# Optimization experiments

Measured on AMD Instinct MI355X. Metric: run time of the kernel, lower is better.

The kernel has to match this reference:

```python
import jax, jax.numpy as jnp
import numpy as np

BSZ, S, F, K, PI = 32, 4096, 512, 4, 1


def setup_inputs() -> dict:
    key = jax.random.key(0)
    ks = jax.random.split(key, 5)
    x = jax.random.normal(ks[0], (BSZ, S, F), dtype=jnp.float32)
    s = 1.0 / np.float32(np.sqrt(F))
    Wu = jax.random.normal(ks[1], (F, F), dtype=jnp.float32) * s
    P = jax.random.normal(ks[2], (F // K, F), dtype=jnp.float32) * s
    Q = jax.random.normal(ks[3], (F, PI * F), dtype=jnp.float32) * s
    Bb = jax.random.normal(ks[4], (F // K, PI * F), dtype=jnp.float32) * 0.01
    return {"x": x, "Wu": Wu, "P": P, "Q": Q, "Bb": Bb}


def reference(x, Wu, P, Q, Bb):
    # x: [B, S, F]
    B_, S_, F_ = x.shape
    Fk = P.shape[0]          # F // k
    k = F_ // Fk
    piF = Q.shape[1]
    # Ux = relu(x @ Wu): [B, S, F]
    Ux = jax.nn.relu(jnp.einsum('bsf,fg->bsg', x, Wu))
    # KMaxPooling over sequence axis: transpose to [B, F, S], top_k -> [B, F, k]
    topv = jax.lax.top_k(jnp.transpose(Ux, (0, 2, 1)), k)[0]
    # original does a raw reshape [B, F, k] -> [B, k, F] (element order preserved)
    z = topv.reshape(B_, k, F_)
    # P is reshaped in call() from [F/k, F] to [F, F/k]
    P2 = P.reshape(F_, Fk)
    # diag(z_i) @ P2 == z_i[:, None] * P2 -> [B, k, F, F/k], then per-i reshape to [B, F/k, F]
    zp = (z[:, :, :, None] * P2[None, None, :, :]).reshape(B_, k, Fk, F_)
    # @ Q, bias add, relu: [B, k, F/k, pi*F]
    out = jax.nn.relu(jnp.einsum('bkmf,fq->bkmq', zp, Q) + Bb[None, None, :, :])
    # concat over k along axis 1 -> [B, F, pi*F]
    return out.reshape(B_, F_, piF)
```

## Files before the change

### kernel.cpp

```cpp
#include <hip/hip_runtime.h>

#define BSZ   32
#define SEQ   4096
#define FDIM  512
#define KTOP  4
#define FK    128
#define MTOT  (BSZ * SEQ)
#define NCHUNK 32

#define BM2  256
#define BN2  256
#define BK2  64
#define NKT  (FDIM / BK2)

typedef __attribute__((ext_vector_type(8))) short bf16x8;
typedef __attribute__((ext_vector_type(4))) float f32x4;
typedef __attribute__((ext_vector_type(8))) unsigned short u16x8;

typedef __attribute__((address_space(1))) void void_g;
typedef __attribute__((address_space(3))) void void_l;

static __device__ __forceinline__ void load_lds16(const void* g, void* l) {
  __builtin_amdgcn_global_load_lds((void_g*)g, (void_l*)l, 16, 0, 0);
}

static __device__ __forceinline__ unsigned short f2bf(float f) {
  unsigned int u = __float_as_uint(f);
  unsigned int r = (u + 0x7fffu + ((u >> 16) & 1u)) >> 16;
  return (unsigned short)r;
}

static __device__ __forceinline__ void sort2(float& a, float& b) {
  float mx = fmaxf(a, b), mn = fminf(a, b); a = mx; b = mn;
}
static __device__ __forceinline__ void sort4(float& a, float& b, float& c, float& d) {
  sort2(a, b); sort2(c, d); sort2(a, c); sort2(b, d); sort2(b, c);
}
static __device__ __forceinline__ void merge4(float& a, float& b, float& c, float& d,
                                              float e, float f, float g, float h) {
  float m0 = fmaxf(a, h), m1 = fmaxf(b, g), m2 = fmaxf(c, f), m3 = fmaxf(d, e);
  sort2(m0, m2); sort2(m1, m3); sort2(m0, m1); sort2(m2, m3);
  a = m0; b = m1; c = m2; d = m3;
}

__global__ __launch_bounds__(256) void cvt_wuT_kernel(const float* __restrict__ Wu,
                                                      unsigned short* __restrict__ WuT) {
  int nn = blockIdx.x;
  for (int k = threadIdx.x; k < FDIM; k += blockDim.x)
    WuT[(size_t)nn * FDIM + k] = f2bf(Wu[(size_t)k * FDIM + nn]);
}

__global__ __launch_bounds__(256) void compute_R_kernel(const float* __restrict__ P,
                                                        const float* __restrict__ Q,
                                                        float* __restrict__ R) {
  int g = blockIdx.y;
  int q = blockIdx.x * 256 + threadIdx.x;
  __shared__ float p2[FK];
  if (threadIdx.x < FK) p2[threadIdx.x] = P[(size_t)g * FK + threadIdx.x];
  __syncthreads();
  const float* Qb = Q + (size_t)((g & 3) * FK) * FDIM + q;
  float s = 0.f;
#pragma unroll 8
  for (int m = 0; m < FK; ++m) s = fmaf(p2[m], Qb[(size_t)m * FDIM], s);
  R[(size_t)g * FDIM + q] = s;
}

__global__ __launch_bounds__(512, 2) void gemm_topk_kernel(
    const float* __restrict__ X, const unsigned short* __restrict__ Bt,
    float* __restrict__ cand) {
  __shared__ __align__(16) unsigned short As[2][BM2 * BK2];
  __shared__ __align__(16) unsigned short Bs[2][BM2 * BK2];

  const int tid = threadIdx.x;
  const int lane = tid & 63;
  const int w = tid >> 6;
  const int wm = w & 1, wn = w >> 1;

  const int xcd = blockIdx.x & 7;
  const int jj = blockIdx.x >> 3;
  const int t = xcd * 128 + jj;
  const int mtile = t >> 1, ntile = t & 1;
  const int m0 = mtile * BM2, n0 = ntile * BN2;

  const int arow = tid >> 3;
  const int asc = tid & 7;
  const int aswz = (arow & 7) << 4;
  const float* axp[4];
  int aldst[4];
#pragma unroll
  for (int i = 0; i < 4; ++i) {
    const int row = i * 64 + arow;
    axp[i] = X + (size_t)(m0 + row) * FDIM + asc * 8;
    aldst[i] = row * 128 + ((asc * 16) ^ aswz);
  }
  float4 ar[4][2];

#define ALOAD(kt)                                                              \
  {                                                                            \
    _Pragma("unroll") for (int i = 0; i < 4; ++i) {                            \
      const float4* p = (const float4*)(axp[i] + (kt) * BK2);                  \
      ar[i][0] = p[0];                                                         \
      ar[i][1] = p[1];                                                         \
    }                                                                          \
  }

#define AWRITE(buf)                                                            \
  {                                                                            \
    _Pragma("unroll") for (int i = 0; i < 4; ++i) {                            \
      u16x8 o;                                                                 \
      o[0] = f2bf(ar[i][0].x); o[1] = f2bf(ar[i][0].y);                        \
      o[2] = f2bf(ar[i][0].z); o[3] = f2bf(ar[i][0].w);                        \
      o[4] = f2bf(ar[i][1].x); o[5] = f2bf(ar[i][1].y);                        \
      o[6] = f2bf(ar[i][1].z); o[7] = f2bf(ar[i][1].w);                        \
      *(u16x8*)((char*)As[buf] + aldst[i]) = o;                                \
    }                                                                          \
  }

  const char* bsrc[4];
#pragma unroll
  for (int i = 0; i < 4; ++i) {
    int o = i * 8192 + tid * 16;
    int row = o >> 7;
    int colb = (o & 127) ^ ((row & 7) << 4);
    bsrc[i] = (const char*)(Bt + (size_t)(n0 + row) * FDIM) + colb;
  }
  const int ldst = (tid >> 6) * 512;

#define STAGE_B(kt, buf)                                                       \
  {                                                                            \
    _Pragma("unroll") for (int i = 0; i < 4; ++i)                              \
        load_lds16(bsrc[i] + (kt) * 128, (void*)(&Bs[buf][i * 4096 + ldst]));  \
  }

  const int lr = lane & 15;
  const int g16 = lane >> 4;
  const int swz = (lr & 7) << 4;
  const int arow0 = (wm * 128 + lr) * 128;
  const int brow0 = (wn * 64 + lr) * 128;

  f32x4 acc[8][4];
#pragma unroll
  for (int mi = 0; mi < 8; ++mi)
#pragma unroll
    for (int ni = 0; ni < 4; ++ni) acc[mi][ni] = {0.f, 0.f, 0.f, 0.f};

  STAGE_B(0, 0);
  ALOAD(0);
  AWRITE(0);
  __syncthreads();

  for (int kt = 0; kt < NKT; ++kt) {
    const int cur = kt & 1;
    if (kt + 1 < NKT) {
      STAGE_B(kt + 1, cur ^ 1);
      ALOAD(kt + 1);
    }
    const char* Ab = (const char*)As[cur];
    const char* Bb = (const char*)Bs[cur];
#pragma unroll
    for (int kk = 0; kk < 2; ++kk) {
      bf16x8 af[8], bfr[4];
      const int kcol = kk * 64;
#pragma unroll
      for (int mi = 0; mi < 8; ++mi)
        af[mi] = *(const bf16x8*)(Ab + arow0 + mi * 2048 + ((kcol + g16 * 16) ^ swz));
#pragma unroll
      for (int ni = 0; ni < 4; ++ni)
        bfr[ni] = *(const bf16x8*)(Bb + brow0 + ni * 2048 + ((kcol + g16 * 16) ^ swz));
      __builtin_amdgcn_s_setprio(1);
#pragma unroll
      for (int mi = 0; mi < 8; ++mi)
#pragma unroll
        for (int ni = 0; ni < 4; ++ni)
          acc[mi][ni] = __builtin_amdgcn_mfma_f32_16x16x32_bf16(af[mi], bfr[ni],
                                                                acc[mi][ni], 0, 0, 0);
      __builtin_amdgcn_s_setprio(0);
    }
    if (kt + 1 < NKT) {
      AWRITE(cur ^ 1);
      __syncthreads();
    }
  }

  const int mchunk = mtile * 2 + wm;
  const int b = mchunk >> 5;
  const int chunk = mchunk & 31;
#pragma unroll
  for (int ni = 0; ni < 4; ++ni) {
    float a0 = acc[0][ni][0], a1 = acc[0][ni][1], a2 = acc[0][ni][2], a3 = acc[0][ni][3];
    sort4(a0, a1, a2, a3);
#pragma unroll
    for (int mi = 1; mi < 8; ++mi) {
      float b0 = acc[mi][ni][0], b1 = acc[mi][ni][1];
      float b2 = acc[mi][ni][2], b3 = acc[mi][ni][3];
      sort4(b0, b1, b2, b3);
      merge4(a0, a1, a2, a3, b0, b1, b2, b3);
    }
#pragma unroll
    for (int off = 16; off < 64; off <<= 1) {
      float e0 = __shfl_xor(a0, off), e1 = __shfl_xor(a1, off);
      float e2 = __shfl_xor(a2, off), e3 = __shfl_xor(a3, off);
      merge4(a0, a1, a2, a3, e0, e1, e2, e3);
    }
    if (lane < 16) {
      const int f = n0 + wn * 64 + ni * 16 + lane;
      float4 v; v.x = a0; v.y = a1; v.z = a2; v.w = a3;
      *(float4*)(cand + (((size_t)(b * FDIM + f)) * NCHUNK + chunk) * 4) = v;
    }
  }
}

__global__ __launch_bounds__(256) void out_kernel(
    const float* __restrict__ cand, const float* __restrict__ R,
    const float* __restrict__ Bb, float* __restrict__ out) {
  const int row = blockIdx.x * 4 + (threadIdx.x >> 6);
  const int lane = threadIdx.x & 63;
  const int b = row >> 9, ff = row & 511;
  const int m2 = ff & 127;

  const float4 cv = *(const float4*)(cand +
      (((size_t)(b * FDIM + ff)) * NCHUNK + (lane & 31)) * 4);
  float t0 = cv.x, t1 = cv.y, t2 = cv.z, t3 = cv.w;
#pragma unroll
  for (int off = 1; off < 32; off <<= 1) {
    float e0 = __shfl_xor(t0, off), e1 = __shfl_xor(t1, off);
    float e2 = __shfl_xor(t2, off), e3 = __shfl_xor(t3, off);
    merge4(t0, t1, t2, t3, e0, e1, e2, e3);
  }
  t0 = fmaxf(t0, 0.f); t1 = fmaxf(t1, 0.f); t2 = fmaxf(t2, 0.f); t3 = fmaxf(t3, 0.f);

  const float* R0 = R + (size_t)(4 * m2) * FDIM;
  const float* Bbr = Bb + (size_t)m2 * FDIM;
  float* ob = out + (size_t)row * FDIM;
#pragma unroll
  for (int jq = 0; jq < 8; ++jq) {
    const int q = jq * 64 + lane;
    float s = Bbr[q];
    s = fmaf(t0, R0[q], s);
    s = fmaf(t1, R0[FDIM + q], s);
    s = fmaf(t2, R0[2 * FDIM + q], s);
    s = fmaf(t3, R0[3 * FDIM + q], s);
    ob[q] = s > 0.f ? s : 0.f;
  }
}

extern "C" void kernel_launch(void* const* d_in, const int* in_sizes, int n_in,
                              void* d_out, int out_size, void* d_ws, size_t ws_size,
                              hipStream_t stream) {
  const float* x  = (const float*)d_in[0];
  const float* Wu = (const float*)d_in[1];
  const float* P  = (const float*)d_in[2];
  const float* Q  = (const float*)d_in[3];
  const float* Bb = (const float*)d_in[4];
  float* out = (float*)d_out;

  char* ws = (char*)d_ws;
  unsigned short* wuT = (unsigned short*)(ws);
  float*          R   = (float*)(ws + 524288L);
  float*          cand= (float*)(ws + 1572864L);

  hipLaunchKernelGGL(cvt_wuT_kernel, dim3(512), dim3(256), 0, stream, Wu, wuT);
  hipLaunchKernelGGL(compute_R_kernel, dim3(2, 512), dim3(256), 0, stream, P, Q, R);
  hipLaunchKernelGGL(gemm_topk_kernel, dim3(1024), dim3(512), 0, stream, x, wuT, cand);
  hipLaunchKernelGGL(out_kernel, dim3(BSZ * FDIM / 4), dim3(256), 0, stream, cand, R, Bb, out);
}
```

Measured before the change: 148.6 us.

## Prefetch A two k-tiles ahead with double register sets and fine-grained waits

Restructures the GEMM main loop into a manually unrolled two-stage pipeline. Two register sets for the fp32 A tile let global loads for tile kt+2 be in flight while tile kt is computed. The full __syncthreads is replaced by explicit vmcnt/lgkmcnt waits plus s_barrier, so B direct-to-LDS loads can stay outstanding across the barrier. This aims to hide global-load latency, at the cost of higher register pressure and fragile, hand-counted waitcnt values.

```diff
diff --git a/kernel.cpp b/kernel.cpp
--- a/kernel.cpp
+++ b/kernel.cpp
@@ -93,25 +93,25 @@
     axp[i] = X + (size_t)(m0 + row) * FDIM + asc * 8;
     aldst[i] = row * 128 + ((asc * 16) ^ aswz);
   }
-  float4 ar[4][2];
-
-#define ALOAD(kt)                                                              \
+  float4 arA[4][2], arB[4][2];
+
+#define ALOADS(set, kt)                                                        \
   {                                                                            \
     _Pragma("unroll") for (int i = 0; i < 4; ++i) {                            \
       const float4* p = (const float4*)(axp[i] + (kt) * BK2);                  \
-      ar[i][0] = p[0];                                                         \
-      ar[i][1] = p[1];                                                         \
+      set[i][0] = p[0];                                                        \
+      set[i][1] = p[1];                                                        \
     }                                                                          \
   }
 
-#define AWRITE(buf)                                                            \
+#define AWRITES(set, buf)                                                      \
   {                                                                            \
     _Pragma("unroll") for (int i = 0; i < 4; ++i) {                            \
       u16x8 o;                                                                 \
-      o[0] = f2bf(ar[i][0].x); o[1] = f2bf(ar[i][0].y);                        \
-      o[2] = f2bf(ar[i][0].z); o[3] = f2bf(ar[i][0].w);                        \
-      o[4] = f2bf(ar[i][1].x); o[5] = f2bf(ar[i][1].y);                        \
-      o[6] = f2bf(ar[i][1].z); o[7] = f2bf(ar[i][1].w);                        \
+      o[0] = f2bf(set[i][0].x); o[1] = f2bf(set[i][0].y);                      \
+      o[2] = f2bf(set[i][0].z); o[3] = f2bf(set[i][0].w);                      \
+      o[4] = f2bf(set[i][1].x); o[5] = f2bf(set[i][1].y);                      \
+      o[6] = f2bf(set[i][1].z); o[7] = f2bf(set[i][1].w);                      \
       *(u16x8*)((char*)As[buf] + aldst[i]) = o;                                \
     }                                                                          \
   }
@@ -144,41 +144,60 @@
 #pragma unroll
     for (int ni = 0; ni < 4; ++ni) acc[mi][ni] = {0.f, 0.f, 0.f, 0.f};
 
+#define COMPUTE(b)                                                             \
+  {                                                                            \
+    const char* Ap = (const char*)As[b];                                       \
+    const char* Bp = (const char*)Bs[b];                                       \
+    _Pragma("unroll") for (int kk = 0; kk < 2; ++kk) {                         \
+      bf16x8 af[8], bfr[4];                                                    \
+      const int kcol = kk * 64;                                                \
+      _Pragma("unroll") for (int mi = 0; mi < 8; ++mi)                         \
+          af[mi] = *(const bf16x8*)(Ap + arow0 + mi * 2048 +                   \
+                                    ((kcol + g16 * 16) ^ swz));                \
+      _Pragma("unroll") for (int ni = 0; ni < 4; ++ni)                         \
+          bfr[ni] = *(const bf16x8*)(Bp + brow0 + ni * 2048 +                  \
+                                     ((kcol + g16 * 16) ^ swz));               \
+      __builtin_amdgcn_s_setprio(1);                                           \
+      _Pragma("unroll") for (int mi = 0; mi < 8; ++mi)                         \
+          _Pragma("unroll") for (int ni = 0; ni < 4; ++ni)                     \
+              acc[mi][ni] = __builtin_amdgcn_mfma_f32_16x16x32_bf16(           \
+                  af[mi], bfr[ni], acc[mi][ni], 0, 0, 0);                      \
+      __builtin_amdgcn_s_setprio(0);                                           \
+    }                                                                          \
+  }
+
+#define WAIT_BAR(n)                                                            \
+  asm volatile("s_waitcnt vmcnt(" #n ") lgkmcnt(0)" ::: "memory");             \
+  __builtin_amdgcn_s_barrier();                                                \
+  __builtin_amdgcn_sched_barrier(0);
+
+  ALOADS(arA, 0);
+  AWRITES(arA, 0);
   STAGE_B(0, 0);
-  ALOAD(0);
-  AWRITE(0);
-  __syncthreads();
-
-  for (int kt = 0; kt < NKT; ++kt) {
-    const int cur = kt & 1;
-    if (kt + 1 < NKT) {
-      STAGE_B(kt + 1, cur ^ 1);
-      ALOAD(kt + 1);
-    }
-    const char* Ab = (const char*)As[cur];
-    const char* Bb = (const char*)Bs[cur];
-#pragma unroll
-    for (int kk = 0; kk < 2; ++kk) {
-      bf16x8 af[8], bfr[4];
-      const int kcol = kk * 64;
-#pragma unroll
-      for (int mi = 0; mi < 8; ++mi)
-        af[mi] = *(const bf16x8*)(Ab + arow0 + mi * 2048 + ((kcol + g16 * 16) ^ swz));
-#pragma unroll
-      for (int ni = 0; ni < 4; ++ni)
-        bfr[ni] = *(const bf16x8*)(Bb + brow0 + ni * 2048 + ((kcol + g16 * 16) ^ swz));
-      __builtin_amdgcn_s_setprio(1);
-#pragma unroll
-      for (int mi = 0; mi < 8; ++mi)
-#pragma unroll
-        for (int ni = 0; ni < 4; ++ni)
-          acc[mi][ni] = __builtin_amdgcn_mfma_f32_16x16x32_bf16(af[mi], bfr[ni],
-                                                                acc[mi][ni], 0, 0, 0);
-      __builtin_amdgcn_s_setprio(0);
-    }
-    if (kt + 1 < NKT) {
-      AWRITE(cur ^ 1);
-      __syncthreads();
+  ALOADS(arB, 1);
+  WAIT_BAR(8);
+
+#pragma unroll 1
+  for (int ktp = 0; ktp < 4; ++ktp) {
+    {
+      const int kt = 2 * ktp;
+      STAGE_B(kt + 1, 1);
+      if (ktp < 3) ALOADS(arA, kt + 2);
+      COMPUTE(0);
+      AWRITES(arB, 1);
+      if (ktp < 3) { WAIT_BAR(8); } else { WAIT_BAR(0); }
+    }
+    {
+      const int kt = 2 * ktp + 1;
+      if (ktp < 3) {
+        STAGE_B(kt + 1, 0);
+        ALOADS(arB, kt + 2);
+      }
+      COMPUTE(1);
+      if (ktp < 3) {
+        AWRITES(arA, 0);
+        WAIT_BAR(8);
+      }
     }
   }
 
```

Result: slower. 328.2 us (+120.8%).
